# Performance work log

Hardware: AMD Instinct MI355X
Metric: run time of the kernel (lower is better)

Reference implementation:

```python
import jax, jax.numpy as jnp
import numpy as np

H = 4096          # hidden_size
I = 14336         # intermediate_size
SC = int(0.3 * I) # beta * I -> size of cached x_topk (4300)
HC = int(0.05 * I)# gamma * I -> helper top-k count (716)


def setup_inputs() -> dict:
    key = jax.random.key(0)
    ks = jax.random.split(key, 7)
    s = 0.02
    return {
        "x": jax.random.normal(ks[0], (1, 1, H), dtype=jnp.float32),
        "x_topk": jax.random.randint(ks[1], (SC,), 0, I, dtype=jnp.int64),
        "gate_w": jax.random.normal(ks[2], (I, H), dtype=jnp.float32) * s,
        "up_w": jax.random.normal(ks[3], (I, H), dtype=jnp.float32) * s,
        "down_w": jax.random.normal(ks[4], (H, I), dtype=jnp.float32) * s,
        "helper_w1": jax.random.normal(ks[5], (1024, H), dtype=jnp.float32) * s,
        "helper_w2": jax.random.normal(ks[6], (I, 1024), dtype=jnp.float32) * s,
    }


def reference(x, x_topk, gate_w, up_w, down_w, helper_w1, helper_w2):
    # --- sparsity predictor (SimpleLinearModel): two bias-free linears ---
    h = (x @ helper_w1.T) @ helper_w2.T                       # [1,1,I]
    up_mask_index = jax.lax.top_k(h.reshape(-1), HC)[1]       # [HC]

    # --- combine cached core indices with predicted indices, dedup ---
    combined = jnp.concatenate([x_topk.astype(jnp.int32),
                                up_mask_index.astype(jnp.int32)])  # [SC+HC]
    K = combined.shape[0]
    uniq = jnp.unique(combined, size=K, fill_value=I)         # padded with I
    valid = (uniq < I)                                        # [K] bool
    idx = jnp.where(valid, uniq, 0)                           # safe gather idx

    # --- gather weight rows/columns, reduced gated-MLP matmul ---
    gate_f = gate_w[idx]                                      # [K,H]
    up_f = up_w[idx]                                          # [K,H]
    gate_out = jnp.einsum('bsh,kh->bsk', x, gate_f)           # [1,1,K]
    up_out = jnp.einsum('bsh,kh->bsk', x, up_f)               # [1,1,K]
    tv = jax.nn.silu(gate_out) * up_out                       # act_fn = SiLU
    tv = tv * valid.astype(tv.dtype)                          # zero padded dups

    down_f = down_w[:, idx]                                   # [H,K]
    down_value = jnp.einsum('bsk,hk->bsh', tv, down_f)        # [1,1,H]
    return down_value
```

## Files before the change

kernel.cpp:

```cpp
#include <hip/hip_runtime.h>
#include <math.h>

#define H_DIM 4096
#define I_DIM 14336
#define HB_DIM 1024
#define SC_K 4300
#define HC_K 716

typedef float floatx4 __attribute__((ext_vector_type(4)));

__device__ __forceinline__ unsigned sortable(float f) {
    unsigned u = __float_as_uint(f);
    return (u & 0x80000000u) ? ~u : (u | 0x80000000u);
}

__device__ __forceinline__ floatx4 ntload4(const float* p) {
    return __builtin_nontemporal_load((const floatx4*)p);
}

__device__ __forceinline__ void compute_tv_row(const float* __restrict__ x,
                                               const float* __restrict__ gate_w,
                                               const float* __restrict__ up_w,
                                               float* __restrict__ tv, int row, int lane) {
    const float* gr = gate_w + (size_t)row * H_DIM;
    const float* ur = up_w + (size_t)row * H_DIM;
    float gs = 0.f, us = 0.f;
#pragma unroll 4
    for (int c = 0; c < H_DIM; c += 256) {
        int cc = c + lane * 4;
        float4 xv = *(const float4*)(x + cc);
        floatx4 g = ntload4(gr + cc);
        floatx4 u = ntload4(ur + cc);
        gs += g.x * xv.x + g.y * xv.y + g.z * xv.z + g.w * xv.w;
        us += u.x * xv.x + u.y * xv.y + u.z * xv.z + u.w * xv.w;
    }
#pragma unroll
    for (int o = 32; o >= 1; o >>= 1) {
        gs += __shfl_xor(gs, o);
        us += __shfl_xor(us, o);
    }
    if (lane == 0) {
        float s = gs / (1.f + expf(-gs));
        tv[row] = s * us;
    }
}

__global__ __launch_bounds__(256) void k1_h1_gateup(
    const float* __restrict__ x, const float* __restrict__ hw1,
    const int* __restrict__ x_topk, const float* __restrict__ gate_w,
    const float* __restrict__ up_w, float* __restrict__ h1,
    float* __restrict__ tv) {
    int wid = threadIdx.x >> 6, lane = threadIdx.x & 63;
    int b = blockIdx.x;
    if (b < 256) {
        int row = b * 4 + wid;
        const float* mr = hw1 + (size_t)row * H_DIM;
        float s = 0.f;
#pragma unroll 4
        for (int c = 0; c < H_DIM; c += 256) {
            int cc = c + lane * 4;
            floatx4 m = ntload4(mr + cc);
            float4 v = *(const float4*)(x + cc);
            s += m.x * v.x + m.y * v.y + m.z * v.z + m.w * v.w;
        }
#pragma unroll
        for (int o = 32; o >= 1; o >>= 1) s += __shfl_xor(s, o);
        if (lane == 0) h1[row] = s;
    } else {
        int gw = (b - 256) * 4 + wid;
        if (gw < SC_K) {
            int idx = x_topk[gw];
            if ((unsigned)idx < (unsigned)I_DIM)
                compute_tv_row(x, gate_w, up_w, tv, idx, lane);
        }
    }
}

__global__ __launch_bounds__(256) void k2_h(
    const float* __restrict__ h1, const float* __restrict__ hw2,
    float* __restrict__ hbuf) {
    int wid = threadIdx.x >> 6, lane = threadIdx.x & 63;
    int row = blockIdx.x * 4 + wid;
    const float* mr = hw2 + (size_t)row * HB_DIM;
    float s = 0.f;
#pragma unroll
    for (int c = 0; c < HB_DIM; c += 256) {
        int cc = c + lane * 4;
        floatx4 m = ntload4(mr + cc);
        float4 v = *(const float4*)(h1 + cc);
        s += m.x * v.x + m.y * v.y + m.z * v.z + m.w * v.w;
    }
#pragma unroll
    for (int o = 32; o >= 1; o >>= 1) s += __shfl_xor(s, o);
    if (lane == 0) hbuf[row] = s;
}

__global__ __launch_bounds__(1024) void select_kernel(
    const float* __restrict__ h, const int* __restrict__ x_topk,
    float* __restrict__ tv, int* __restrict__ rlist, int* __restrict__ rcount) {
    __shared__ unsigned hist[16][256];
    __shared__ unsigned wpart[4];
    __shared__ unsigned bitT[448], bitS[448];
    __shared__ int s_d, s_above, s_tie_cnt, s_rc;
    __shared__ int tie_idx[2048];
    int tid = threadIdx.x;
    int lane = tid & 63, wid = tid >> 6;

    unsigned key[14];
#pragma unroll
    for (int j = 0; j < 14; ++j) key[j] = sortable(h[j * 1024 + tid]);

    if (tid < 448) { bitT[tid] = 0; bitS[tid] = 0; }
    if (tid == 0) { s_tie_cnt = 0; s_rc = 0; }
    __syncthreads();

    for (int k = tid; k < SC_K; k += 1024) {
        int idx = x_topk[k];
        if ((unsigned)idx < (unsigned)I_DIM) atomicOr(&bitT[idx >> 5], 1u << (idx & 31));
    }

    unsigned prefix = 0;
    int above = 0;

    for (int p = 0; p < 4; ++p) {
        int s = 24 - 8 * p;
        {
            unsigned* hp = &hist[0][0];
            for (int i = tid; i < 4096; i += 1024) hp[i] = 0;
        }
        __syncthreads();
#pragma unroll
        for (int j = 0; j < 14; ++j) {
            unsigned u = key[j];
            bool in_sub = (p == 0) || ((u >> (s + 8)) == (prefix >> (s + 8)));
            if (in_sub) atomicAdd(&hist[wid][(u >> s) & 0xFF], 1u);
        }
        __syncthreads();
        unsigned cnt = 0, incl = 0;
        if (tid < 256) {
#pragma unroll
            for (int w = 0; w < 16; ++w) cnt += hist[w][tid];
        }
        incl = cnt;
#pragma unroll
        for (int o = 1; o < 64; o <<= 1) {
            unsigned v = __shfl_up(incl, o);
            if (lane >= o) incl += v;
        }
        if (tid < 256 && lane == 63) wpart[wid] = incl;
        __syncthreads();
        if (tid < 256) {
            unsigned add = 0;
            for (int w2 = 0; w2 < wid; ++w2) add += wpart[w2];
            incl += add;
            unsigned total = wpart[0] + wpart[1] + wpart[2] + wpart[3];
            unsigned suf = total - incl;
            unsigned needk = (unsigned)(HC_K - above);
            if (suf < needk && suf + cnt >= needk) {
                s_d = tid;
                s_above = above + (int)suf;
            }
        }
        __syncthreads();
        prefix |= ((unsigned)s_d) << s;
        above = s_above;
        __syncthreads();
    }

    unsigned T = prefix;
    int need2 = HC_K - above;

#pragma unroll
    for (int j = 0; j < 14; ++j) {
        unsigned u = key[j];
        int i = j * 1024 + tid;
        if (u > T) atomicOr(&bitS[i >> 5], 1u << (i & 31));
        else if (u == T) {
            int pp = atomicAdd(&s_tie_cnt, 1);
            if (pp < 2048) tie_idx[pp] = i;
        }
    }
    __syncthreads();
    int C = s_tie_cnt;
    if (C <= 2048) {
        for (int m = tid; m < C; m += 1024) {
            int my = tie_idx[m];
            int rank = 0;
            for (int j = 0; j < C; ++j) rank += (tie_idx[j] < my) ? 1 : 0;
            if (rank < need2) atomicOr(&bitS[my >> 5], 1u << (my & 31));
        }
    } else if (tid == 0) {
        int left = need2;
        for (int i = 0; i < I_DIM && left > 0; ++i)
            if (sortable(h[i]) == T) { atomicOr(&bitS[i >> 5], 1u << (i & 31)); --left; }
    }
    __syncthreads();

#pragma unroll
    for (int j = 0; j < 14; ++j) {
        int i = j * 1024 + tid;
        bool t = (bitT[i >> 5] >> (i & 31)) & 1u;
        bool sl = (bitS[i >> 5] >> (i & 31)) & 1u;
        if (!t) {
            if (sl) {
                int pp = atomicAdd(&s_rc, 1);
                rlist[pp] = i;
            } else {
                tv[i] = 0.f;
            }
        }
    }
    __syncthreads();
    if (tid == 0) *rcount = s_rc;
}

__global__ __launch_bounds__(256) void k3_residual(
    const float* __restrict__ x, const float* __restrict__ gate_w,
    const float* __restrict__ up_w, const int* __restrict__ rlist,
    const int* __restrict__ rcount, float* __restrict__ tv) {
    int wid = threadIdx.x >> 6, lane = threadIdx.x & 63;
    int gw = blockIdx.x * 4 + wid;
    if (gw < *rcount) compute_tv_row(x, gate_w, up_w, tv, rlist[gw], lane);
}

__global__ __launch_bounds__(256) void k4_down(
    const float* __restrict__ tv, const float* __restrict__ down_w,
    float* __restrict__ out) {
    int wid = threadIdx.x >> 6, lane = threadIdx.x & 63;
    int row = blockIdx.x * 4 + wid;
    const float* mr = down_w + (size_t)row * I_DIM;
    float s = 0.f;
#pragma unroll 4
    for (int c = 0; c < I_DIM; c += 256) {
        int cc = c + lane * 4;
        floatx4 m = ntload4(mr + cc);
        float4 v = *(const float4*)(tv + cc);
        s += m.x * v.x + m.y * v.y + m.z * v.z + m.w * v.w;
    }
#pragma unroll
    for (int o = 32; o >= 1; o >>= 1) s += __shfl_xor(s, o);
    if (lane == 0) out[row] = s;
}

extern "C" void kernel_launch(void* const* d_in, const int* in_sizes, int n_in,
                              void* d_out, int out_size, void* d_ws, size_t ws_size,
                              hipStream_t stream) {
    const float* x      = (const float*)d_in[0];
    const int*   x_topk = (const int*)d_in[1];
    const float* gate_w = (const float*)d_in[2];
    const float* up_w   = (const float*)d_in[3];
    const float* down_w = (const float*)d_in[4];
    const float* hw1    = (const float*)d_in[5];
    const float* hw2    = (const float*)d_in[6];
    float* out = (float*)d_out;

    float* ws    = (float*)d_ws;
    float* h1    = ws;
    float* hbuf  = ws + 1024;
    float* tv    = ws + 1024 + I_DIM;
    int*   rlist = (int*)(ws + 1024 + 2 * I_DIM);
    int*   rcount = rlist + 768;

    k1_h1_gateup<<<256 + (SC_K + 3) / 4, 256, 0, stream>>>(x, hw1, x_topk, gate_w,
                                                           up_w, h1, tv);
    k2_h<<<I_DIM / 4, 256, 0, stream>>>(h1, hw2, hbuf);
    select_kernel<<<1, 1024, 0, stream>>>(hbuf, x_topk, tv, rlist, rcount);
    k3_residual<<<(HC_K + 3) / 4, 256, 0, stream>>>(x, gate_w, up_w, rlist, rcount, tv);
    k4_down<<<H_DIM / 4, 256, 0, stream>>>(tv, down_w, out);
}
```

Before: 99.94 us.

## Move gate/up row computation into helper-layer-2 kernel with per-row membership scan

The cached gate/up dot products move out of the helper layer-1 kernel and into the layer-2 kernel. There, one wave per intermediate row scans all of x_topk to test membership and computes that row only if it is present. This deduplicates repeated indices, which were previously written with redundant loads, and balances the two kernels' work. The cost is a 4300-element index scan in each of 14336 waves. The kernel with the larger grid also lengthens the dependency chain before selection.

After: 114.7 us. 1.15x slower.

```diff
diff --git a/kernel.cpp b/kernel.cpp
--- a/kernel.cpp
+++ b/kernel.cpp
@@ -45,54 +45,52 @@
     }
 }
 
-__global__ __launch_bounds__(256) void k1_h1_gateup(
+__global__ __launch_bounds__(256) void k1_h1(
     const float* __restrict__ x, const float* __restrict__ hw1,
-    const int* __restrict__ x_topk, const float* __restrict__ gate_w,
-    const float* __restrict__ up_w, float* __restrict__ h1,
-    float* __restrict__ tv) {
+    float* __restrict__ h1) {
+    int wid = threadIdx.x >> 6, lane = threadIdx.x & 63;
+    int row = blockIdx.x * 4 + wid;
+    const float* mr = hw1 + (size_t)row * H_DIM;
+    float s = 0.f;
+#pragma unroll 4
+    for (int c = 0; c < H_DIM; c += 256) {
+        int cc = c + lane * 4;
+        floatx4 m = ntload4(mr + cc);
+        float4 v = *(const float4*)(x + cc);
+        s += m.x * v.x + m.y * v.y + m.z * v.z + m.w * v.w;
+    }
+#pragma unroll
+    for (int o = 32; o >= 1; o >>= 1) s += __shfl_xor(s, o);
+    if (lane == 0) h1[row] = s;
+}
+
+__global__ __launch_bounds__(256) void k2_h_gateup(
+    const float* __restrict__ h1, const float* __restrict__ hw2,
+    float* __restrict__ hbuf, const int* __restrict__ x_topk,
+    const float* __restrict__ x, const float* __restrict__ gate_w,
+    const float* __restrict__ up_w, float* __restrict__ tv) {
     int wid = threadIdx.x >> 6, lane = threadIdx.x & 63;
     int b = blockIdx.x;
-    if (b < 256) {
+    if (b < I_DIM / 4) {
         int row = b * 4 + wid;
-        const float* mr = hw1 + (size_t)row * H_DIM;
+        const float* mr = hw2 + (size_t)row * HB_DIM;
         float s = 0.f;
-#pragma unroll 4
-        for (int c = 0; c < H_DIM; c += 256) {
+#pragma unroll
+        for (int c = 0; c < HB_DIM; c += 256) {
             int cc = c + lane * 4;
             floatx4 m = ntload4(mr + cc);
-            float4 v = *(const float4*)(x + cc);
+            float4 v = *(const float4*)(h1 + cc);
             s += m.x * v.x + m.y * v.y + m.z * v.z + m.w * v.w;
         }
 #pragma unroll
         for (int o = 32; o >= 1; o >>= 1) s += __shfl_xor(s, o);
-        if (lane == 0) h1[row] = s;
+        if (lane == 0) hbuf[row] = s;
     } else {
-        int gw = (b - 256) * 4 + wid;
-        if (gw < SC_K) {
-            int idx = x_topk[gw];
-            if ((unsigned)idx < (unsigned)I_DIM)
-                compute_tv_row(x, gate_w, up_w, tv, idx, lane);
-        }
-    }
-}
-
-__global__ __launch_bounds__(256) void k2_h(
-    const float* __restrict__ h1, const float* __restrict__ hw2,
-    float* __restrict__ hbuf) {
-    int wid = threadIdx.x >> 6, lane = threadIdx.x & 63;
-    int row = blockIdx.x * 4 + wid;
-    const float* mr = hw2 + (size_t)row * HB_DIM;
-    float s = 0.f;
-#pragma unroll
-    for (int c = 0; c < HB_DIM; c += 256) {
-        int cc = c + lane * 4;
-        floatx4 m = ntload4(mr + cc);
-        float4 v = *(const float4*)(h1 + cc);
-        s += m.x * v.x + m.y * v.y + m.z * v.z + m.w * v.w;
-    }
-#pragma unroll
-    for (int o = 32; o >= 1; o >>= 1) s += __shfl_xor(s, o);
-    if (lane == 0) hbuf[row] = s;
+        int row = (b - I_DIM / 4) * 4 + wid;
+        bool found = false;
+        for (int k = lane; k < SC_K; k += 64) found |= (x_topk[k] == row);
+        if (__any(found)) compute_tv_row(x, gate_w, up_w, tv, row, lane);
+    }
 }
 
 __global__ __launch_bounds__(1024) void select_kernel(
@@ -261,9 +259,9 @@
     int*   rlist = (int*)(ws + 1024 + 2 * I_DIM);
     int*   rcount = rlist + 768;
 
-    k1_h1_gateup<<<256 + (SC_K + 3) / 4, 256, 0, stream>>>(x, hw1, x_topk, gate_w,
-                                                           up_w, h1, tv);
-    k2_h<<<I_DIM / 4, 256, 0, stream>>>(h1, hw2, hbuf);
+    k1_h1<<<HB_DIM / 4, 256, 0, stream>>>(x, hw1, h1);
+    k2_h_gateup<<<2 * (I_DIM / 4), 256, 0, stream>>>(h1, hw2, hbuf, x_topk, x,
+                                                     gate_w, up_w, tv);
     select_kernel<<<1, 1024, 0, stream>>>(hbuf, x_topk, tv, rlist, rcount);
     k3_residual<<<(HC_K + 3) / 4, 256, 0, stream>>>(x, gate_w, up_w, rlist, rcount, tv);
     k4_down<<<H_DIM / 4, 256, 0, stream>>>(tv, down_w, out);
```

## Fuse select and residual kernels with spin-wait flag, move tv zeroing into k2

Applied to the files above, without the earlier changes.

Merges the single-block top-k select kernel and the residual gate/up kernel into one launch. Block 0 builds the selection list and publishes the count with a release store, while 45 worker blocks spin on that flag and then compute the residual rows. Zeroing of the non-cached tv entries moves into extra blocks of the k2 helper kernel. This removes one kernel launch and takes the zeroing off the serial select path, but relies on all blocks being co-resident to avoid deadlock. Worker blocks also burn cycles spinning while block 0 runs.

Measured after the change: 110.2 us. +10.3%, slower.

```diff
diff --git a/kernel.cpp b/kernel.cpp
--- a/kernel.cpp
+++ b/kernel.cpp
@@ -76,151 +76,184 @@
     }
 }
 
-__global__ __launch_bounds__(256) void k2_h(
+__global__ __launch_bounds__(256) void k2_h_zero(
     const float* __restrict__ h1, const float* __restrict__ hw2,
-    float* __restrict__ hbuf) {
-    int wid = threadIdx.x >> 6, lane = threadIdx.x & 63;
-    int row = blockIdx.x * 4 + wid;
-    const float* mr = hw2 + (size_t)row * HB_DIM;
-    float s = 0.f;
-#pragma unroll
-    for (int c = 0; c < HB_DIM; c += 256) {
-        int cc = c + lane * 4;
-        floatx4 m = ntload4(mr + cc);
-        float4 v = *(const float4*)(h1 + cc);
-        s += m.x * v.x + m.y * v.y + m.z * v.z + m.w * v.w;
-    }
-#pragma unroll
-    for (int o = 32; o >= 1; o >>= 1) s += __shfl_xor(s, o);
-    if (lane == 0) hbuf[row] = s;
-}
-
-__global__ __launch_bounds__(1024) void select_kernel(
+    float* __restrict__ hbuf, const int* __restrict__ x_topk,
+    float* __restrict__ tv, int* __restrict__ rcount) {
+    int b = blockIdx.x;
+    if (b < I_DIM / 4) {
+        int wid = threadIdx.x >> 6, lane = threadIdx.x & 63;
+        int row = b * 4 + wid;
+        const float* mr = hw2 + (size_t)row * HB_DIM;
+        float s = 0.f;
+#pragma unroll
+        for (int c = 0; c < HB_DIM; c += 256) {
+            int cc = c + lane * 4;
+            floatx4 m = ntload4(mr + cc);
+            float4 v = *(const float4*)(h1 + cc);
+            s += m.x * v.x + m.y * v.y + m.z * v.z + m.w * v.w;
+        }
+#pragma unroll
+        for (int o = 32; o >= 1; o >>= 1) s += __shfl_xor(s, o);
+        if (lane == 0) hbuf[row] = s;
+    } else {
+        int zb = b - I_DIM / 4;
+        int base = zb * 1024;
+        if (zb == 0 && threadIdx.x == 0)
+            __hip_atomic_store(rcount, -1, __ATOMIC_RELEASE, __HIP_MEMORY_SCOPE_AGENT);
+        __shared__ unsigned bits[32];
+        if (threadIdx.x < 32) bits[threadIdx.x] = 0;
+        __syncthreads();
+        for (int k = threadIdx.x; k < SC_K; k += 256) {
+            int idx = x_topk[k] - base;
+            if ((unsigned)idx < 1024u) atomicOr(&bits[idx >> 5], 1u << (idx & 31));
+        }
+        __syncthreads();
+        for (int r = threadIdx.x; r < 1024; r += 256) {
+            if (!((bits[r >> 5] >> (r & 31)) & 1u)) tv[base + r] = 0.f;
+        }
+    }
+}
+
+__global__ __launch_bounds__(1024) void k3_select_residual(
     const float* __restrict__ h, const int* __restrict__ x_topk,
-    float* __restrict__ tv, int* __restrict__ rlist, int* __restrict__ rcount) {
-    __shared__ unsigned hist[16][256];
-    __shared__ unsigned wpart[4];
-    __shared__ unsigned bitT[448], bitS[448];
-    __shared__ int s_d, s_above, s_tie_cnt, s_rc;
-    __shared__ int tie_idx[2048];
+    const float* __restrict__ x, const float* __restrict__ gate_w,
+    const float* __restrict__ up_w, float* __restrict__ tv,
+    int* __restrict__ rlist, int* __restrict__ rcount) {
     int tid = threadIdx.x;
     int lane = tid & 63, wid = tid >> 6;
 
-    unsigned key[14];
-#pragma unroll
-    for (int j = 0; j < 14; ++j) key[j] = sortable(h[j * 1024 + tid]);
-
-    if (tid < 448) { bitT[tid] = 0; bitS[tid] = 0; }
-    if (tid == 0) { s_tie_cnt = 0; s_rc = 0; }
-    __syncthreads();
-
-    for (int k = tid; k < SC_K; k += 1024) {
-        int idx = x_topk[k];
-        if ((unsigned)idx < (unsigned)I_DIM) atomicOr(&bitT[idx >> 5], 1u << (idx & 31));
-    }
-
-    unsigned prefix = 0;
-    int above = 0;
-
-    for (int p = 0; p < 4; ++p) {
-        int s = 24 - 8 * p;
-        {
-            unsigned* hp = &hist[0][0];
-            for (int i = tid; i < 4096; i += 1024) hp[i] = 0;
-        }
-        __syncthreads();
+    if (blockIdx.x == 0) {
+        __shared__ unsigned hist[16][256];
+        __shared__ unsigned wpart[4];
+        __shared__ unsigned bitT[448], bitS[448];
+        __shared__ int s_d, s_above, s_tie_cnt, s_rc;
+        __shared__ int tie_idx[2048];
+
+        unsigned key[14];
+#pragma unroll
+        for (int j = 0; j < 14; ++j) key[j] = sortable(h[j * 1024 + tid]);
+
+        if (tid < 448) { bitT[tid] = 0; bitS[tid] = 0; }
+        if (tid == 0) { s_tie_cnt = 0; s_rc = 0; }
+        __syncthreads();
+
+        for (int k = tid; k < SC_K; k += 1024) {
+            int idx = x_topk[k];
+            if ((unsigned)idx < (unsigned)I_DIM) atomicOr(&bitT[idx >> 5], 1u << (idx & 31));
+        }
+
+        unsigned prefix = 0;
+        int above = 0;
+
+        for (int p = 0; p < 4; ++p) {
+            int s = 24 - 8 * p;
+            {
+                unsigned* hp = &hist[0][0];
+                for (int i = tid; i < 4096; i += 1024) hp[i] = 0;
+            }
+            __syncthreads();
+#pragma unroll
+            for (int j = 0; j < 14; ++j) {
+                unsigned u = key[j];
+                bool in_sub = (p == 0) || ((u >> (s + 8)) == (prefix >> (s + 8)));
+                if (in_sub) atomicAdd(&hist[wid][(u >> s) & 0xFF], 1u);
+            }
+            __syncthreads();
+            unsigned cnt = 0, incl = 0;
+            if (tid < 256) {
+#pragma unroll
+                for (int w = 0; w < 16; ++w) cnt += hist[w][tid];
+            }
+            incl = cnt;
+#pragma unroll
+            for (int o = 1; o < 64; o <<= 1) {
+                unsigned v = __shfl_up(incl, o);
+                if (lane >= o) incl += v;
+            }
+            if (tid < 256 && lane == 63) wpart[wid] = incl;
+            __syncthreads();
+            if (tid < 256) {
+                unsigned add = 0;
+                for (int w2 = 0; w2 < wid; ++w2) add += wpart[w2];
+                incl += add;
+                unsigned total = wpart[0] + wpart[1] + wpart[2] + wpart[3];
+                unsigned suf = total - incl;
+                unsigned needk = (unsigned)(HC_K - above);
+                if (suf < needk && suf + cnt >= needk) {
+                    s_d = tid;
+                    s_above = above + (int)suf;
+                }
+            }
+            __syncthreads();
+            prefix |= ((unsigned)s_d) << s;
+            above = s_above;
+            __syncthreads();
+        }
+
+        unsigned T = prefix;
+        int need2 = HC_K - above;
+
 #pragma unroll
         for (int j = 0; j < 14; ++j) {
             unsigned u = key[j];
-            bool in_sub = (p == 0) || ((u >> (s + 8)) == (prefix >> (s + 8)));
-            if (in_sub) atomicAdd(&hist[wid][(u >> s) & 0xFF], 1u);
-        }
-        __syncthreads();
-        unsigned cnt = 0, incl = 0;
-        if (tid < 256) {
-#pragma unroll
-            for (int w = 0; w < 16; ++w) cnt += hist[w][tid];
-        }
-        incl = cnt;
-#pragma unroll
-        for (int o = 1; o < 64; o <<= 1) {
-            unsigned v = __shfl_up(incl, o);
-            if (lane >= o) incl += v;
-        }
-        if (tid < 256 && lane == 63) wpart[wid] = incl;
-        __syncthreads();
-        if (tid < 256) {
-            unsigned add = 0;
-            for (int w2 = 0; w2 < wid; ++w2) add += wpart[w2];
-            incl += add;
-            unsigned total = wpart[0] + wpart[1] + wpart[2] + wpart[3];
-            unsigned suf = total - incl;
-            unsigned needk = (unsigned)(HC_K - above);
-            if (suf < needk && suf + cnt >= needk) {
-                s_d = tid;
-                s_above = above + (int)suf;
-            }
-        }
-        __syncthreads();
-        prefix |= ((unsigned)s_d) << s;
-        above = s_above;
-        __syncthreads();
-    }
-
-    unsigned T = prefix;
-    int need2 = HC_K - above;
-
-#pragma unroll
-    for (int j = 0; j < 14; ++j) {
-        unsigned u = key[j];
-        int i = j * 1024 + tid;
-        if (u > T) atomicOr(&bitS[i >> 5], 1u << (i & 31));
-        else if (u == T) {
-            int pp = atomicAdd(&s_tie_cnt, 1);
-            if (pp < 2048) tie_idx[pp] = i;
-        }
-    }
-    __syncthreads();
-    int C = s_tie_cnt;
-    if (C <= 2048) {
-        for (int m = tid; m < C; m += 1024) {
-            int my = tie_idx[m];
-            int rank = 0;
-            for (int j = 0; j < C; ++j) rank += (tie_idx[j] < my) ? 1 : 0;
-            if (rank < need2) atomicOr(&bitS[my >> 5], 1u << (my & 31));
-        }
-    } else if (tid == 0) {
-        int left = need2;
-        for (int i = 0; i < I_DIM && left > 0; ++i)
-            if (sortable(h[i]) == T) { atomicOr(&bitS[i >> 5], 1u << (i & 31)); --left; }
-    }
-    __syncthreads();
-
-#pragma unroll
-    for (int j = 0; j < 14; ++j) {
-        int i = j * 1024 + tid;
-        bool t = (bitT[i >> 5] >> (i & 31)) & 1u;
-        bool sl = (bitS[i >> 5] >> (i & 31)) & 1u;
-        if (!t) {
-            if (sl) {
+            int i = j * 1024 + tid;
+            if (u > T) atomicOr(&bitS[i >> 5], 1u << (i & 31));
+            else if (u == T) {
+                int pp = atomicAdd(&s_tie_cnt, 1);
+                if (pp < 2048) tie_idx[pp] = i;
+            }
+        }
+        __syncthreads();
+        int C = s_tie_cnt;
+        if (C <= 2048) {
+            for (int m = tid; m < C; m += 1024) {
+                int my = tie_idx[m];
+                int rank = 0;
+                for (int j = 0; j < C; ++j) rank += (tie_idx[j] < my) ? 1 : 0;
+                if (rank < need2) atomicOr(&bitS[my >> 5], 1u << (my & 31));
+            }
+        } else if (tid == 0) {
+            int left = need2;
+            for (int i = 0; i < I_DIM && left > 0; ++i)
+                if (sortable(h[i]) == T) { atomicOr(&bitS[i >> 5], 1u << (i & 31)); --left; }
+        }
+        __syncthreads();
+
+#pragma unroll
+        for (int j = 0; j < 14; ++j) {
+            int i = j * 1024 + tid;
+            bool t = (bitT[i >> 5] >> (i & 31)) & 1u;
+            bool sl = (bitS[i >> 5] >> (i & 31)) & 1u;
+            if (sl && !t) {
                 int pp = atomicAdd(&s_rc, 1);
-                rlist[pp] = i;
-            } else {
-                tv[i] = 0.f;
-            }
-        }
-    }
-    __syncthreads();
-    if (tid == 0) *rcount = s_rc;
-}
-
-__global__ __launch_bounds__(256) void k3_residual(
-    const float* __restrict__ x, const float* __restrict__ gate_w,
-    const float* __restrict__ up_w, const int* __restrict__ rlist,
-    const int* __restrict__ rcount, float* __restrict__ tv) {
-    int wid = threadIdx.x >> 6, lane = threadIdx.x & 63;
-    int gw = blockIdx.x * 4 + wid;
-    if (gw < *rcount) compute_tv_row(x, gate_w, up_w, tv, rlist[gw], lane);
+                __hip_atomic_store(&rlist[pp], i, __ATOMIC_RELAXED, __HIP_MEMORY_SCOPE_AGENT);
+            }
+        }
+        __syncthreads();
+        if (tid == 0) {
+            __threadfence();
+            __hip_atomic_store(rcount, s_rc, __ATOMIC_RELEASE, __HIP_MEMORY_SCOPE_AGENT);
+        }
+    } else {
+        __shared__ int w_rc;
+        if (tid == 0) {
+            int rc;
+            while ((rc = __hip_atomic_load(rcount, __ATOMIC_ACQUIRE,
+                                           __HIP_MEMORY_SCOPE_AGENT)) < 0)
+                __builtin_amdgcn_s_sleep(16);
+            w_rc = rc;
+        }
+        __syncthreads();
+        int rc = w_rc;
+        int r = (blockIdx.x - 1) * 16 + wid;
+        if (r < rc) {
+            int row = __hip_atomic_load(&rlist[r], __ATOMIC_RELAXED,
+                                        __HIP_MEMORY_SCOPE_AGENT);
+            if ((unsigned)row < (unsigned)I_DIM)
+                compute_tv_row(x, gate_w, up_w, tv, row, lane);
+        }
+    }
 }
 
 __global__ __launch_bounds__(256) void k4_down(
@@ -263,8 +296,8 @@
 
     k1_h1_gateup<<<256 + (SC_K + 3) / 4, 256, 0, stream>>>(x, hw1, x_topk, gate_w,
                                                            up_w, h1, tv);
-    k2_h<<<I_DIM / 4, 256, 0, stream>>>(h1, hw2, hbuf);
-    select_kernel<<<1, 1024, 0, stream>>>(hbuf, x_topk, tv, rlist, rcount);
-    k3_residual<<<(HC_K + 3) / 4, 256, 0, stream>>>(x, gate_w, up_w, rlist, rcount, tv);
+    k2_h_zero<<<I_DIM / 4 + 14, 256, 0, stream>>>(h1, hw2, hbuf, x_topk, tv, rcount);
+    k3_select_residual<<<46, 1024, 0, stream>>>(hbuf, x_topk, x, gate_w, up_w,
+                                                tv, rlist, rcount);
     k4_down<<<H_DIM / 4, 256, 0, stream>>>(tv, down_w, out);
 }
```
